# Optimization experiments

Hardware: AMD Instinct MI355X
Metric: run time of the kernel (lower is better)

## Reference

```python
import jax, jax.numpy as jnp
import numpy as np

B, NK, NQ, DK, DQ, H, DV = 16, 256, 256, 256, 256, 128, 256
MASK_VAL = -1000000.0

def setup_inputs() -> dict:
    key = jax.random.key(0)
    ks = jax.random.split(key, 7)
    return {
        "key": jax.random.normal(ks[0], (B, NK, DK), dtype=jnp.float32),
        "query": jax.random.normal(ks[1], (B, NQ, DQ), dtype=jnp.float32),
        "value": jax.random.normal(ks[2], (B, NQ, DV), dtype=jnp.float32),
        "valid_lens": jax.random.randint(ks[3], (B,), 1, NQ + 1, dtype=jnp.int32),
        "Wk": jax.random.normal(ks[4], (DK, H), dtype=jnp.float32) / np.sqrt(DK),
        "Wq": jax.random.normal(ks[5], (DQ, H), dtype=jnp.float32) / np.sqrt(DQ),
        "wv": jax.random.normal(ks[6], (H,), dtype=jnp.float32) / np.sqrt(H),
    }

def reference(key, query, value, valid_lens, Wk, Wq, wv):
    k = key @ Wk                      # (B, NK, H)
    q = query @ Wq                    # (B, NQ, H)
    # note: original unsqueezes key at dim 2, query at dim 1 -> (B, NK, NQ, H)
    feature = jnp.tanh(k[:, :, None, :] + q[:, None, :, :])
    scores = jnp.einsum('bkqh,h->bkq', feature, wv)   # (B, NK, NQ)
    # mask along last (query) axis per batch, as repeat_interleave does
    pos = jnp.arange(scores.shape[-1])[None, None, :]
    masked = jnp.where(pos < valid_lens[:, None, None], scores, MASK_VAL)
    attn = jax.nn.softmax(masked, axis=-1)            # (B, NK, NQ)
    return jnp.einsum('bkq,bqd->bkd', attn, value)    # (B, NK, DV)
```

## Files before the change

### kernel.cpp

```cpp
#include <hip/hip_runtime.h>

#define B_   16
#define NK_  256
#define NQ_  256
#define DK_  256
#define H_   128
#define DV_  256

#define C2X 2.8853900817779268f
#define L2E 1.4426950408889634f

typedef float f4 __attribute__((ext_vector_type(4)));

__device__ __forceinline__ float exp2_fast(float x) { return __builtin_amdgcn_exp2f(x); }
__device__ __forceinline__ float rcp_fast(float x)  { return __builtin_amdgcn_rcpf(x); }

__global__ __launch_bounds__(256) void proj_kernel(
    const float* __restrict__ key, const float* __restrict__ query,
    const float* __restrict__ Wk,  const float* __restrict__ Wq,
    float* __restrict__ kfc, float* __restrict__ qfcT)
{
    __shared__ alignas(16) float A_s[32 * 256];
    __shared__ alignas(16) float W_s[64 * 128];

    const int blk = blockIdx.x;
    const int tid = threadIdx.x;
    const bool isQ = blk >= 128;
    const int rb = (blk & 127) * 32;

    const float* __restrict__ A = isQ ? query : key;
    const float* __restrict__ W = isQ ? Wq : Wk;

    {
        const f4* src = (const f4*)(A + (size_t)rb * DK_);
        f4* dst = (f4*)A_s;
#pragma unroll
        for (int j = 0; j < 8; ++j) dst[tid + 256 * j] = src[tid + 256 * j];
    }

    const int rg = (tid >> 5) * 4;
    const int c4 = (tid & 31) * 4;

    f4 acc[4];
#pragma unroll
    for (int r = 0; r < 4; ++r) acc[r] = (f4){0.f, 0.f, 0.f, 0.f};

    for (int kc = 0; kc < DK_; kc += 64) {
        __syncthreads();
        {
            const f4* wsrc = (const f4*)(W + (size_t)kc * H_);
            f4* wdst = (f4*)W_s;
#pragma unroll
            for (int j = 0; j < 8; ++j) wdst[tid + 256 * j] = wsrc[tid + 256 * j];
        }
        __syncthreads();
#pragma unroll 2
        for (int k = 0; k < 64; k += 4) {
            f4 w0 = *(const f4*)(W_s + (k + 0) * H_ + c4);
            f4 w1 = *(const f4*)(W_s + (k + 1) * H_ + c4);
            f4 w2 = *(const f4*)(W_s + (k + 2) * H_ + c4);
            f4 w3 = *(const f4*)(W_s + (k + 3) * H_ + c4);
#pragma unroll
            for (int r = 0; r < 4; ++r) {
                f4 a = *(const f4*)(A_s + (rg + r) * 256 + kc + k);
                acc[r] += a[0] * w0;
                acc[r] += a[1] * w1;
                acc[r] += a[2] * w2;
                acc[r] += a[3] * w3;
            }
        }
    }

    if (!isQ) {
        float* dst = kfc + (size_t)(rb + rg) * H_ + c4;
#pragma unroll
        for (int r = 0; r < 4; ++r)
            *(f4*)(dst + (size_t)r * H_) = C2X * acc[r];
    } else {
        const int b  = rb >> 8;
        const int q0 = (rb & 255) + rg;
#pragma unroll
        for (int cc = 0; cc < 4; ++cc) {
            f4 o;
            o[0] = C2X * acc[0][cc]; o[1] = C2X * acc[1][cc];
            o[2] = C2X * acc[2][cc]; o[3] = C2X * acc[3][cc];
            *(f4*)(qfcT + ((size_t)b * H_ + c4 + cc) * NQ_ + q0) = o;
        }
    }
}

__global__ __launch_bounds__(256) void attn_kernel(
    const float* __restrict__ kfc, const float* __restrict__ qfcT,
    const float* __restrict__ value, const int* __restrict__ vlens,
    const float* __restrict__ wv, float* __restrict__ out)
{
    __shared__ alignas(16) float kf_s[4 * 132];
    __shared__ alignas(16) float wv2_s[128];
    __shared__ alignas(16) float sc_s[4 * 260];
    __shared__ alignas(16) float at4_s[256 * 4];
    __shared__ alignas(16) float red_s[16 * 256];

    const int x   = blockIdx.x;
    const int qu  = x >> 8;
    const int xi  = x & 255;
    const int b   = (xi + (qu << 2)) & 15;
    const int kt  = (xi >> 4) + (qu << 4);
    const int k0  = kt << 2;
    const int rot = ((xi >> 4) + qu) & 3;
    const int tid = threadIdx.x;
    const int valid = vlens[b];

    if (tid < 128) {
        const int k = tid >> 5, h4 = tid & 31;
        f4 v = ((const f4*)(kfc + ((size_t)(b * NK_ + k0 + k)) * H_))[h4];
        *(f4*)(kf_s + k * 132 + (h4 << 2)) = v;
    }
    if (tid < 32) {
        f4 w = ((const f4*)wv)[tid];
        ((f4*)wv2_s)[tid] = 2.f * w;
    }
    __syncthreads();

    float sumwv;
    {
        f4 sw = {0.f, 0.f, 0.f, 0.f};
#pragma unroll
        for (int i = 0; i < 32; ++i) sw += ((const f4*)wv)[i];
        sumwv = (sw[0] + sw[1]) + (sw[2] + sw[3]);
    }

    {
        const int g     = tid & 3;
        const int range = ((tid >> 6) + rot) & 3;
        const int q4    = ((((tid >> 2) & 15)) << 2) + (range << 6);
        if (q4 < valid) {
            const float* qbase = qfcT + (size_t)b * (H_ * NQ_) + q4;
            const float* kb = kf_s + g * 132;
            float acc0 = 0.f, acc1 = 0.f, acc2 = 0.f, acc3 = 0.f;
            for (int h = 0; h < H_; h += 4) {
                f4 w4 = *(const f4*)(wv2_s + h);
                f4 kA = *(const f4*)(kb + h);
                f4 qq[4];
                qq[0] = *(const f4*)(qbase + (size_t)(h + 0) * NQ_);
                qq[1] = *(const f4*)(qbase + (size_t)(h + 1) * NQ_);
                qq[2] = *(const f4*)(qbase + (size_t)(h + 2) * NQ_);
                qq[3] = *(const f4*)(qbase + (size_t)(h + 3) * NQ_);
#pragma unroll
                for (int j = 0; j < 4; ++j) {
                    const float kj = kA[j];
                    const float wj = w4[j];
                    const f4 qv = qq[j];
                    float r;
                    r = rcp_fast(exp2_fast(kj + qv[0]) + 1.f); acc0 = fmaf(wj, r, acc0);
                    r = rcp_fast(exp2_fast(kj + qv[1]) + 1.f); acc1 = fmaf(wj, r, acc1);
                    r = rcp_fast(exp2_fast(kj + qv[2]) + 1.f); acc2 = fmaf(wj, r, acc2);
                    r = rcp_fast(exp2_fast(kj + qv[3]) + 1.f); acc3 = fmaf(wj, r, acc3);
                }
            }
            f4 s;
            s[0] = sumwv - acc0; s[1] = sumwv - acc1;
            s[2] = sumwv - acc2; s[3] = sumwv - acc3;
            *(f4*)(sc_s + g * 260 + q4) = s;
        }
    }
    __syncthreads();

    {
        const int k   = tid >> 6;
        const int sub = tid & 63;
        const float* row = sc_s + k * 260;
        float ev[4];
        float m = -3.0e38f;
#pragma unroll
        for (int j = 0; j < 4; ++j) {
            const int q = sub + (j << 6);
            ev[j] = (q < valid) ? row[q] : -3.0e38f;
            m = fmaxf(m, ev[j]);
        }
#pragma unroll
        for (int off = 32; off >= 1; off >>= 1)
            m = fmaxf(m, __shfl_xor(m, off, 64));
        float ssum = 0.f;
#pragma unroll
        for (int j = 0; j < 4; ++j) {
            const int q = sub + (j << 6);
            const float e = (q < valid) ? exp2_fast(L2E * (ev[j] - m)) : 0.f;
            ev[j] = e;
            ssum += e;
        }
#pragma unroll
        for (int off = 32; off >= 1; off >>= 1)
            ssum += __shfl_xor(ssum, off, 64);
        const float inv = rcp_fast(ssum);
#pragma unroll
        for (int j = 0; j < 4; ++j) {
            const int q = sub + (j << 6);
            if (q < valid) at4_s[(q << 2) + k] = ev[j] * inv;
        }
    }
    __syncthreads();

    {
        const int rq = tid >> 6;
        const int d4 = (tid & 63) << 2;
        const float* vb = value + (size_t)b * (NQ_ * DV_) + d4;
        f4 o0 = {0.f,0.f,0.f,0.f}, o1 = o0, o2 = o0, o3 = o0;
#pragma unroll 4
        for (int q = rq; q < valid; q += 4) {
            f4 v  = *(const f4*)(vb + (size_t)q * DV_);
            f4 a4 = *(const f4*)(at4_s + (q << 2));
            o0 += a4[0] * v;
            o1 += a4[1] * v;
            o2 += a4[2] * v;
            o3 += a4[3] * v;
        }
        float* rs = red_s + (rq << 10) + d4;
        *(f4*)(rs + 0)    = o0;
        *(f4*)(rs + 256)  = o1;
        *(f4*)(rs + 512)  = o2;
        *(f4*)(rs + 768)  = o3;
    }
    __syncthreads();

    {
        const int k  = tid >> 6;
        const int d4 = (tid & 63) << 2;
        const float* rs = red_s + (k << 8) + d4;
        f4 o = *(const f4*)(rs) + *(const f4*)(rs + 1024)
             + *(const f4*)(rs + 2048) + *(const f4*)(rs + 3072);
        *(f4*)(out + ((size_t)(b * NK_ + k0 + k)) * DV_ + d4) = o;
    }
}

extern "C" void kernel_launch(void* const* d_in, const int* in_sizes, int n_in,
                              void* d_out, int out_size, void* d_ws, size_t ws_size,
                              hipStream_t stream)
{
    const float* key   = (const float*)d_in[0];
    const float* query = (const float*)d_in[1];
    const float* value = (const float*)d_in[2];
    const int*   vlens = (const int*)  d_in[3];
    const float* Wk    = (const float*)d_in[4];
    const float* Wq    = (const float*)d_in[5];
    const float* wv    = (const float*)d_in[6];
    float* outp = (float*)d_out;

    float* kfc  = (float*)d_ws;
    float* qfcT = kfc + (size_t)B_ * NK_ * H_;

    hipLaunchKernelGGL(proj_kernel, dim3(256), dim3(256), 0, stream,
                       key, query, Wk, Wq, kfc, qfcT);
    hipLaunchKernelGGL(attn_kernel, dim3(1024), dim3(256), 0, stream,
                       kfc, qfcT, value, vlens, wv, outp);
}
```

Measured before the change: 118.3 us.

## Precompute exponentials of projections to factor tanh into product form

```diff
diff --git a/kernel.cpp b/kernel.cpp
--- a/kernel.cpp
+++ b/kernel.cpp
@@ -9,6 +9,7 @@
 
 #define C2X 2.8853900817779268f
 #define L2E 1.4426950408889634f
+#define MASKV -1.0e5f
 
 typedef float f4 __attribute__((ext_vector_type(4)));
 
@@ -18,7 +19,7 @@
 __global__ __launch_bounds__(256) void proj_kernel(
     const float* __restrict__ key, const float* __restrict__ query,
     const float* __restrict__ Wk,  const float* __restrict__ Wq,
-    float* __restrict__ kfc, float* __restrict__ qfcT)
+    float* __restrict__ kfE, float* __restrict__ qE4)
 {
     __shared__ alignas(16) float A_s[32 * 256];
     __shared__ alignas(16) float W_s[64 * 128];
@@ -72,31 +73,35 @@
     }
 
     if (!isQ) {
-        float* dst = kfc + (size_t)(rb + rg) * H_ + c4;
-#pragma unroll
-        for (int r = 0; r < 4; ++r)
-            *(f4*)(dst + (size_t)r * H_) = C2X * acc[r];
+        float* dst = kfE + (size_t)(rb + rg) * H_ + c4;
+#pragma unroll
+        for (int r = 0; r < 4; ++r) {
+            f4 o;
+#pragma unroll
+            for (int cc = 0; cc < 4; ++cc) o[cc] = exp2_fast(C2X * acc[r][cc]);
+            *(f4*)(dst + (size_t)r * H_) = o;
+        }
     } else {
         const int b  = rb >> 8;
         const int q0 = (rb & 255) + rg;
-#pragma unroll
-        for (int cc = 0; cc < 4; ++cc) {
+        f4* dst = (f4*)qE4 + ((size_t)(b * 32 + (c4 >> 2))) * NQ_ + q0;
+#pragma unroll
+        for (int r = 0; r < 4; ++r) {
             f4 o;
-            o[0] = C2X * acc[0][cc]; o[1] = C2X * acc[1][cc];
-            o[2] = C2X * acc[2][cc]; o[3] = C2X * acc[3][cc];
-            *(f4*)(qfcT + ((size_t)b * H_ + c4 + cc) * NQ_ + q0) = o;
+#pragma unroll
+            for (int cc = 0; cc < 4; ++cc) o[cc] = exp2_fast(C2X * acc[r][cc]);
+            dst[r] = o;
         }
     }
 }
 
 __global__ __launch_bounds__(256) void attn_kernel(
-    const float* __restrict__ kfc, const float* __restrict__ qfcT,
+    const float* __restrict__ kfE, const float* __restrict__ qE4,
     const float* __restrict__ value, const int* __restrict__ vlens,
     const float* __restrict__ wv, float* __restrict__ out)
 {
     __shared__ alignas(16) float kf_s[4 * 132];
     __shared__ alignas(16) float wv2_s[128];
-    __shared__ alignas(16) float sc_s[4 * 260];
     __shared__ alignas(16) float at4_s[256 * 4];
     __shared__ alignas(16) float red_s[16 * 256];
 
@@ -106,18 +111,20 @@
     const int b   = (xi + (qu << 2)) & 15;
     const int kt  = (xi >> 4) + (qu << 4);
     const int k0  = kt << 2;
-    const int rot = ((xi >> 4) + qu) & 3;
     const int tid = threadIdx.x;
-    const int valid = vlens[b];
+    const int w   = tid >> 6;
+    const int lane = tid & 63;
+    const int valid  = vlens[b];
+    const int nchunk = (valid + 63) >> 6;
 
     if (tid < 128) {
         const int k = tid >> 5, h4 = tid & 31;
-        f4 v = ((const f4*)(kfc + ((size_t)(b * NK_ + k0 + k)) * H_))[h4];
+        f4 v = ((const f4*)(kfE + ((size_t)(b * NK_ + k0 + k)) * H_))[h4];
         *(f4*)(kf_s + k * 132 + (h4 << 2)) = v;
     }
     if (tid < 32) {
-        f4 w = ((const f4*)wv)[tid];
-        ((f4*)wv2_s)[tid] = 2.f * w;
+        f4 wvv = ((const f4*)wv)[tid];
+        ((f4*)wv2_s)[tid] = 2.f * wvv;
     }
     __syncthreads();
 
@@ -129,74 +136,68 @@
         sumwv = (sw[0] + sw[1]) + (sw[2] + sw[3]);
     }
 
-    {
-        const int g     = tid & 3;
-        const int range = ((tid >> 6) + rot) & 3;
-        const int q4    = ((((tid >> 2) & 15)) << 2) + (range << 6);
-        if (q4 < valid) {
-            const float* qbase = qfcT + (size_t)b * (H_ * NQ_) + q4;
-            const float* kb = kf_s + g * 132;
-            float acc0 = 0.f, acc1 = 0.f, acc2 = 0.f, acc3 = 0.f;
-            for (int h = 0; h < H_; h += 4) {
-                f4 w4 = *(const f4*)(wv2_s + h);
-                f4 kA = *(const f4*)(kb + h);
-                f4 qq[4];
-                qq[0] = *(const f4*)(qbase + (size_t)(h + 0) * NQ_);
-                qq[1] = *(const f4*)(qbase + (size_t)(h + 1) * NQ_);
-                qq[2] = *(const f4*)(qbase + (size_t)(h + 2) * NQ_);
-                qq[3] = *(const f4*)(qbase + (size_t)(h + 3) * NQ_);
+    float accA[4], accB[4];
+#pragma unroll
+    for (int j = 0; j < 4; ++j) { accA[j] = 0.f; accB[j] = 0.f; }
+
+    {
+        const f4* eq0 = (const f4*)qE4 + (size_t)b * (32 * NQ_) + lane;
+        const float* kb = kf_s + w * 132;
+
+        auto run = [&](int NC) {
+            const f4* eqp = eq0;
+#pragma unroll 4
+            for (int h4 = 0; h4 < 32; ++h4) {
+                f4 ek = *(const f4*)(kb + (h4 << 2));
+                f4 w2 = *(const f4*)(wv2_s + (h4 << 2));
 #pragma unroll
                 for (int j = 0; j < 4; ++j) {
-                    const float kj = kA[j];
-                    const float wj = w4[j];
-                    const f4 qv = qq[j];
-                    float r;
-                    r = rcp_fast(exp2_fast(kj + qv[0]) + 1.f); acc0 = fmaf(wj, r, acc0);
-                    r = rcp_fast(exp2_fast(kj + qv[1]) + 1.f); acc1 = fmaf(wj, r, acc1);
-                    r = rcp_fast(exp2_fast(kj + qv[2]) + 1.f); acc2 = fmaf(wj, r, acc2);
-                    r = rcp_fast(exp2_fast(kj + qv[3]) + 1.f); acc3 = fmaf(wj, r, acc3);
+                    if (j >= NC) break;
+                    f4 eq = eqp[j << 6];
+                    float t0 = fmaf(ek[0], eq[0], 1.f);
+                    float t1 = fmaf(ek[1], eq[1], 1.f);
+                    float t2 = fmaf(ek[2], eq[2], 1.f);
+                    float t3 = fmaf(ek[3], eq[3], 1.f);
+                    accA[j] = fmaf(w2[0], rcp_fast(t0), accA[j]);
+                    accB[j] = fmaf(w2[1], rcp_fast(t1), accB[j]);
+                    accA[j] = fmaf(w2[2], rcp_fast(t2), accA[j]);
+                    accB[j] = fmaf(w2[3], rcp_fast(t3), accB[j]);
                 }
+                eqp += NQ_;
             }
-            f4 s;
-            s[0] = sumwv - acc0; s[1] = sumwv - acc1;
-            s[2] = sumwv - acc2; s[3] = sumwv - acc3;
-            *(f4*)(sc_s + g * 260 + q4) = s;
-        }
-    }
-    __syncthreads();
-
-    {
-        const int k   = tid >> 6;
-        const int sub = tid & 63;
-        const float* row = sc_s + k * 260;
-        float ev[4];
-        float m = -3.0e38f;
+        };
+        switch (nchunk) {
+            case 1: run(1); break;
+            case 2: run(2); break;
+            case 3: run(3); break;
+            default: run(4); break;
+        }
+    }
+
+    {
+        float s[4];
 #pragma unroll
         for (int j = 0; j < 4; ++j) {
-            const int q = sub + (j << 6);
-            ev[j] = (q < valid) ? row[q] : -3.0e38f;
-            m = fmaxf(m, ev[j]);
-        }
+            const int q = (j << 6) + lane;
+            s[j] = (j < nchunk && q < valid) ? (sumwv - (accA[j] + accB[j])) : MASKV;
+        }
+        float m = fmaxf(fmaxf(s[0], s[1]), fmaxf(s[2], s[3]));
 #pragma unroll
         for (int off = 32; off >= 1; off >>= 1)
             m = fmaxf(m, __shfl_xor(m, off, 64));
         float ssum = 0.f;
 #pragma unroll
         for (int j = 0; j < 4; ++j) {
-            const int q = sub + (j << 6);
-            const float e = (q < valid) ? exp2_fast(L2E * (ev[j] - m)) : 0.f;
-            ev[j] = e;
-            ssum += e;
+            s[j] = exp2_fast(L2E * (s[j] - m));
+            ssum += s[j];
         }
 #pragma unroll
         for (int off = 32; off >= 1; off >>= 1)
             ssum += __shfl_xor(ssum, off, 64);
         const float inv = rcp_fast(ssum);
 #pragma unroll
-        for (int j = 0; j < 4; ++j) {
-            const int q = sub + (j << 6);
-            if (q < valid) at4_s[(q << 2) + k] = ev[j] * inv;
-        }
+        for (int j = 0; j < 4; ++j)
+            at4_s[(((j << 6) + lane) << 2) + w] = s[j] * inv;
     }
     __syncthreads();
 
@@ -245,11 +246,11 @@
     const float* wv    = (const float*)d_in[6];
     float* outp = (float*)d_out;
 
-    float* kfc  = (float*)d_ws;
-    float* qfcT = kfc + (size_t)B_ * NK_ * H_;
+    float* kfE = (float*)d_ws;
+    float* qE4 = kfE + (size_t)B_ * NK_ * H_;
 
     hipLaunchKernelGGL(proj_kernel, dim3(256), dim3(256), 0, stream,
-                       key, query, Wk, Wq, kfc, qfcT);
+                       key, query, Wk, Wq, kfE, qE4);
     hipLaunchKernelGGL(attn_kernel, dim3(1024), dim3(256), 0, stream,
-                       kfc, qfcT, value, vlens, wv, outp);
+                       kfE, qE4, value, vlens, wv, outp);
 }
```

Measured after the change: 102.9 us. -13.0%, faster.
